# Optimization experiments

Measured on AMD Instinct MI355X. Metric: run time of the kernel, lower is better.

Reference implementation:

```python
import jax, jax.numpy as jnp
import numpy as np

N = 16384      # number of points (pixels)
C = 64         # value channels of U
D_REF = 5      # bilateral reference feature dim (xy + rgb)


def setup_inputs() -> dict:
    key = jax.random.key(0)
    k1, k2 = jax.random.split(key)
    U = jax.random.normal(k1, (N, C), dtype=jnp.float32)
    ref = jax.random.normal(k2, (N, D_REF), dtype=jnp.float32)
    return {"U": U, "ref": ref}


def reference(U, ref):
    # Gaussian filtering on reference features (exact form of the LSH-approx filter):
    #   out[i] = sum_j exp(-0.5 * ||ref_i - ref_j||^2) * U[j]  -  U[i]
    sq = jnp.sum(ref * ref, axis=-1)                      # [N]
    d2 = sq[:, None] + sq[None, :] - 2.0 * (ref @ ref.T)  # [N, N] squared distances
    K = jnp.exp(-0.5 * jnp.maximum(d2, 0.0))              # [N, N] Gaussian kernel
    return K @ U - U                                       # [N, C]
```

## Files before the change

### kernel.cpp

```cpp
#include <hip/hip_runtime.h>
#include <hip/hip_bf16.h>
#include <stdint.h>

#define N_PTS 16384
#define C_CH  64
#define D_REF 5
#define LOG2E 1.44269504088896340736f
#define IBLOCKS 64

typedef __attribute__((ext_vector_type(8))) short bf16x8;
typedef __attribute__((ext_vector_type(4))) float f32x4;

__device__ __forceinline__ unsigned short bf16rn(float v) {
    unsigned u = __builtin_bit_cast(unsigned, v) + 0x8000u;
    return (unsigned short)(u >> 16);
}
__device__ __forceinline__ float bf16tof(unsigned x) {
    return __builtin_bit_cast(float, x << 16);
}
__device__ __forceinline__ unsigned pack2bf16(float lo, float hi) {
    unsigned a = __builtin_bit_cast(unsigned, lo) + 0x8000u;
    unsigned b = __builtin_bit_cast(unsigned, hi) + 0x8000u;
    return __builtin_amdgcn_perm(b, a, 0x07060302u);
}
__device__ __forceinline__ unsigned cvt2(float lo, float hi) {
#if __has_builtin(__builtin_amdgcn_cvt_pk_bf16_f32)
    typedef __attribute__((ext_vector_type(2))) __bf16 bf162_t;
    bf162_t r = __builtin_amdgcn_cvt_pk_bf16_f32(lo, hi);
    return __builtin_bit_cast(unsigned, r);
#else
    return pack2bf16(lo, hi);
#endif
}
__device__ __forceinline__ float fast_exp2(float x) {
#if __has_builtin(__builtin_amdgcn_exp2f)
    return __builtin_amdgcn_exp2f(x);
#else
    return exp2f(x);
#endif
}

__device__ __forceinline__ void dma16(const unsigned short* g, unsigned short* l) {
#if __has_builtin(__builtin_amdgcn_global_load_lds)
    __builtin_amdgcn_global_load_lds(
        (const __attribute__((address_space(1))) unsigned int*)g,
        (__attribute__((address_space(3))) unsigned int*)l, 16, 0, 0);
#else
    const int lane = threadIdx.x & 63;
    *(uint4*)(l + lane * 8) = *(const uint4*)(g);
#endif
}

__global__ __launch_bounds__(256) void prep_all(
    const float* __restrict__ U, const float* __restrict__ ref,
    unsigned short* __restrict__ packA, unsigned short* __restrict__ packB,
    unsigned short* __restrict__ utPack)
{
    __shared__ unsigned short tile[64 * 80];
    const int bid = blockIdx.x;
    const int t   = threadIdx.x;

    if (bid < 512) {
        const int gid  = bid * 256 + t;
        const int half = gid >> 16;
        const int id   = gid & 0xFFFF;
        const int tile16 = id >> 6;
        const int lane = id & 63;
        const int q    = lane >> 4;
        const int m    = lane & 15;
        const int p = half ? (tile16 * 16 + m)
                           : ((tile16 >> 1) * 32 + (m >> 2) * 8 + (m & 3) + (tile16 & 1) * 4);

        const float* r = ref + (size_t)p * D_REF;
        float rv[5];
        float sq = 0.f;
#pragma unroll
        for (int d = 0; d < 5; ++d) { rv[d] = r[d]; sq += rv[d] * rv[d]; }
        const float h = -0.5f * LOG2E * sq;

        unsigned short bh[5], bl[5];
#pragma unroll
        for (int d = 0; d < 5; ++d) {
            const float base = half ? rv[d] * LOG2E : rv[d];
            bh[d] = bf16rn(base);
            bl[d] = bf16rn(base - bf16tof(bh[d]));
        }
        const unsigned short hh  = bf16rn(h);
        const unsigned short hl  = bf16rn(h - bf16tof(hh));
        const unsigned short one = 0x3F80;

        unsigned short outv[8];
#pragma unroll
        for (int tt = 0; tt < 8; ++tt) {
            const int k = q * 8 + tt;
            unsigned short v = 0;
            if (!half) {
                if      (k < 5)   v = bh[k];
                else if (k < 10)  v = bh[k - 5];
                else if (k < 15)  v = bl[k - 10];
                else if (k == 15) v = hh;
                else if (k == 16) v = hl;
                else if (k <= 18) v = one;
            } else {
                if      (k < 5)   v = bh[k];
                else if (k < 10)  v = bl[k - 5];
                else if (k < 15)  v = bh[k - 10];
                else if (k <= 16) v = one;
                else if (k == 17) v = hh;
                else if (k == 18) v = hl;
            }
            outv[tt] = v;
        }
        unsigned short* dst = (half ? packB : packA) + ((size_t)tile16 * 64 + lane) * 8;
        *(uint4*)dst = *(uint4*)outv;
    } else {
        const int b  = bid - 512;
        const int j0 = b * 64;
        const int c  = t & 63;
        const int jb = t >> 6;
#pragma unroll
        for (int k = 0; k < 16; ++k) {
            const int jr = jb + k * 4;
            tile[c * 80 + jr] = bf16rn(U[(size_t)(j0 + jr) * C_CH + c]);
        }
        __syncthreads();
#pragma unroll
        for (int rep = 0; rep < 2; ++rep) {
            const int id   = rep * 256 + t;
            const int lane = id & 63;
            const int ct   = (id >> 6) & 3;
            const int kt   = id >> 8;
            const int m    = lane & 15;
            const int q    = lane >> 4;
            const int cc   = ct * 16 + m;
            const int jloc = kt * 32 + q * 8;
            const uint4 frag = *(const uint4*)&tile[cc * 80 + jloc];
            const int jtile  = b * 2 + kt;
            *(uint4*)&utPack[(((size_t)jtile * 4 + ct) * 64 + lane) * 8] = frag;
        }
    }
}

template<int JS>
__global__ __launch_bounds__(256, 3) void lsh_main(
    const float* __restrict__ U,
    const unsigned short* __restrict__ packA,
    const unsigned short* __restrict__ packB,
    const unsigned short* __restrict__ utPack,
    unsigned short* __restrict__ part,
    float* __restrict__ out,
    int use_part)
{
    constexpr int UNITS  = (N_PTS / JS) / 32;
    constexpr int CUNITS = 8;
    constexpr int NCH    = UNITS / CUNITS;
    __shared__ __align__(16) unsigned short sh[CUNITS * 2048];

    const int t    = threadIdx.x;
    const int lane = t & 63;
    const int wave = t >> 6;
    const int q    = lane >> 4;
    const int m    = lane & 15;

    const int ib = blockIdx.x / JS;
    const int js = blockIdx.x % JS;

    bf16x8 bfrag[4];
#pragma unroll
    for (int s = 0; s < 4; ++s) {
        const int itile = ib * 16 + wave * 4 + s;
        bfrag[s] = *(const bf16x8*)(packB + ((size_t)itile * 64 + lane) * 8);
    }

    f32x4 acc[4][4];
#pragma unroll
    for (int s = 0; s < 4; ++s)
#pragma unroll
        for (int ct = 0; ct < 4; ++ct) acc[s][ct] = (f32x4){0.f, 0.f, 0.f, 0.f};

    const bf16x8 zero8 = {0, 0, 0, 0, 0, 0, 0, 0};
    bf16x8 cs0 = zero8, cs1 = zero8;
    bf16x8 uf[4] = {zero8, zero8, zero8, zero8};

    const unsigned short* pA = packA + ((size_t)js * UNITS) * 1024 + lane * 8;
    bf16x8 ga0 = *(const bf16x8*)pA;
    bf16x8 ga1 = *(const bf16x8*)(pA + 512);

    for (int ch = 0; ch < NCH; ++ch) {
        const unsigned short* srcU = utPack + (size_t)(js * UNITS + ch * CUNITS) * 2048;
        __syncthreads();
#pragma unroll
        for (int r = 0; r < CUNITS; ++r)
            dma16(srcU + (r * 4 + wave) * 512 + lane * 8, sh + (r * 4 + wave) * 512);
        __syncthreads();

#pragma unroll
        for (int u8 = 0; u8 < CUNITS; ++u8) {
            const f32x4 z = (f32x4){0.f, 0.f, 0.f, 0.f};
            f32x4 g0a = __builtin_amdgcn_mfma_f32_16x16x32_bf16(ga0, bfrag[0], z, 0, 0, 0);
            f32x4 g1a = __builtin_amdgcn_mfma_f32_16x16x32_bf16(ga1, bfrag[0], z, 0, 0, 0);
            f32x4 g0b = __builtin_amdgcn_mfma_f32_16x16x32_bf16(ga0, bfrag[1], z, 0, 0, 0);
            f32x4 g1b = __builtin_amdgcn_mfma_f32_16x16x32_bf16(ga1, bfrag[1], z, 0, 0, 0);
#pragma unroll
            for (int ct = 0; ct < 4; ++ct) {
                acc[2][ct] = __builtin_amdgcn_mfma_f32_16x16x32_bf16(uf[ct], cs0, acc[2][ct], 0, 0, 0);
                acc[3][ct] = __builtin_amdgcn_mfma_f32_16x16x32_bf16(uf[ct], cs1, acc[3][ct], 0, 0, 0);
            }
#pragma unroll
            for (int ct = 0; ct < 4; ++ct)
                uf[ct] = *(const bf16x8*)(sh + u8 * 2048 + ct * 512 + lane * 8);
            {
                union { unsigned u[4]; bf16x8 v; } sa, sb;
                sa.u[0] = cvt2(fast_exp2(g0a[0]), fast_exp2(g0a[1]));
                sa.u[1] = cvt2(fast_exp2(g0a[2]), fast_exp2(g0a[3]));
                sa.u[2] = cvt2(fast_exp2(g1a[0]), fast_exp2(g1a[1]));
                sa.u[3] = cvt2(fast_exp2(g1a[2]), fast_exp2(g1a[3]));
                sb.u[0] = cvt2(fast_exp2(g0b[0]), fast_exp2(g0b[1]));
                sb.u[1] = cvt2(fast_exp2(g0b[2]), fast_exp2(g0b[3]));
                sb.u[2] = cvt2(fast_exp2(g1b[0]), fast_exp2(g1b[1]));
                sb.u[3] = cvt2(fast_exp2(g1b[2]), fast_exp2(g1b[3]));
                cs0 = sa.v;
                cs1 = sb.v;
            }
            f32x4 h0a = __builtin_amdgcn_mfma_f32_16x16x32_bf16(ga0, bfrag[2], z, 0, 0, 0);
            f32x4 h1a = __builtin_amdgcn_mfma_f32_16x16x32_bf16(ga1, bfrag[2], z, 0, 0, 0);
            f32x4 h0b = __builtin_amdgcn_mfma_f32_16x16x32_bf16(ga0, bfrag[3], z, 0, 0, 0);
            f32x4 h1b = __builtin_amdgcn_mfma_f32_16x16x32_bf16(ga1, bfrag[3], z, 0, 0, 0);
#pragma unroll
            for (int ct = 0; ct < 4; ++ct) {
                acc[0][ct] = __builtin_amdgcn_mfma_f32_16x16x32_bf16(uf[ct], cs0, acc[0][ct], 0, 0, 0);
                acc[1][ct] = __builtin_amdgcn_mfma_f32_16x16x32_bf16(uf[ct], cs1, acc[1][ct], 0, 0, 0);
            }
            const bf16x8 nga0 = *(const bf16x8*)(pA + 1024);
            const bf16x8 nga1 = *(const bf16x8*)(pA + 1536);
            pA += 1024;
            {
                union { unsigned u[4]; bf16x8 v; } sa, sb;
                sa.u[0] = cvt2(fast_exp2(h0a[0]), fast_exp2(h0a[1]));
                sa.u[1] = cvt2(fast_exp2(h0a[2]), fast_exp2(h0a[3]));
                sa.u[2] = cvt2(fast_exp2(h1a[0]), fast_exp2(h1a[1]));
                sa.u[3] = cvt2(fast_exp2(h1a[2]), fast_exp2(h1a[3]));
                sb.u[0] = cvt2(fast_exp2(h0b[0]), fast_exp2(h0b[1]));
                sb.u[1] = cvt2(fast_exp2(h0b[2]), fast_exp2(h0b[3]));
                sb.u[2] = cvt2(fast_exp2(h1b[0]), fast_exp2(h1b[1]));
                sb.u[3] = cvt2(fast_exp2(h1b[2]), fast_exp2(h1b[3]));
                cs0 = sa.v;
                cs1 = sb.v;
            }
            ga0 = nga0;
            ga1 = nga1;
        }
    }
#pragma unroll
    for (int ct = 0; ct < 4; ++ct) {
        acc[2][ct] = __builtin_amdgcn_mfma_f32_16x16x32_bf16(uf[ct], cs0, acc[2][ct], 0, 0, 0);
        acc[3][ct] = __builtin_amdgcn_mfma_f32_16x16x32_bf16(uf[ct], cs1, acc[3][ct], 0, 0, 0);
    }

    if (use_part) {
        unsigned short* dst = part + ((size_t)js * IBLOCKS + ib) * 16384;
#pragma unroll
        for (int s = 0; s < 4; ++s)
#pragma unroll
            for (int cp = 0; cp < 2; ++cp) {
                uint4 w;
                w.x = cvt2(acc[s][cp*2+0][0], acc[s][cp*2+0][1]);
                w.y = cvt2(acc[s][cp*2+0][2], acc[s][cp*2+0][3]);
                w.z = cvt2(acc[s][cp*2+1][0], acc[s][cp*2+1][1]);
                w.w = cvt2(acc[s][cp*2+1][2], acc[s][cp*2+1][3]);
                *(uint4*)(dst + ((s * 2 + cp) * 256 + t) * 8) = w;
            }
    } else {
#pragma unroll
        for (int s = 0; s < 4; ++s) {
            const int i_glob = ib * 256 + (wave * 4 + s) * 16 + m;
#pragma unroll
            for (int ct = 0; ct < 4; ++ct)
#pragma unroll
                for (int r2 = 0; r2 < 4; ++r2) {
                    const int c = ct * 16 + q * 4 + r2;
                    float val = acc[s][ct][r2];
                    if (js == 0) val -= U[(size_t)i_glob * C_CH + c];
                    atomicAdd(&out[(size_t)i_glob * C_CH + c], val);
                }
        }
    }
}

template<int JS>
__global__ __launch_bounds__(256) void reduce_part(
    const unsigned short* __restrict__ part, const f32x4* __restrict__ Uv,
    f32x4* __restrict__ out)
{
    const int x  = blockIdx.x * 256 + threadIdx.x;
    const int i  = x >> 4;
    const int c4 = (x & 15) * 4;
    const int blk = i >> 8, il = i & 255;
    const int wv = il >> 6, s = (il >> 4) & 3, mm = il & 15;
    const int ct = c4 >> 4, qq = (c4 >> 2) & 3;
    const int cp = ct >> 1, cti = ct & 1;
    const size_t off = (size_t)blk * 16384 +
        (size_t)(((s * 2 + cp) * 256) + (wv * 64 + qq * 16 + mm)) * 8 + cti * 4;
    float s0 = 0.f, s1 = 0.f, s2 = 0.f, s3 = 0.f;
#pragma unroll
    for (int js = 0; js < JS; ++js) {
        const uint2 w = *(const uint2*)(part + (size_t)js * (IBLOCKS * 16384) + off);
        s0 += bf16tof(w.x & 0xFFFFu);
        s1 += bf16tof(w.x >> 16);
        s2 += bf16tof(w.y & 0xFFFFu);
        s3 += bf16tof(w.y >> 16);
    }
    const f32x4 u = Uv[x];
    out[x] = (f32x4){s0 - u[0], s1 - u[1], s2 - u[2], s3 - u[3]};
}

extern "C" void kernel_launch(void* const* d_in, const int* in_sizes, int n_in,
                              void* d_out, int out_size, void* d_ws, size_t ws_size,
                              hipStream_t stream) {
    const float* U   = (const float*)d_in[0];
    const float* ref = (const float*)d_in[1];
    float* out = (float*)d_out;

    unsigned short* utPack = (unsigned short*)d_ws;
    unsigned short* packA  = (unsigned short*)((char*)d_ws + (size_t)2 * 1024 * 1024);
    unsigned short* packB  = (unsigned short*)((char*)d_ws + (size_t)3 * 1024 * 1024);
    unsigned short* part   = (unsigned short*)((char*)d_ws + (size_t)4 * 1024 * 1024);

    const size_t MB = 1024 * 1024;
    prep_all<<<768, 256, 0, stream>>>(U, ref, packA, packB, utPack);

    if (ws_size >= (4 + 2 * 16) * MB) {
        lsh_main<16><<<IBLOCKS * 16, 256, 0, stream>>>(U, packA, packB, utPack,
                                                       part, out, 1);
        reduce_part<16><<<1024, 256, 0, stream>>>(part, (const f32x4*)U, (f32x4*)out);
    } else {
        hipMemsetAsync(d_out, 0, (size_t)out_size * sizeof(float), stream);
        lsh_main<8><<<IBLOCKS * 8, 256, 0, stream>>>(U, packA, packB, utPack,
                                                     part, out, 0);
    }
}
```

Before: 124.1 us.

## Fuse split-K partial reduction into main kernel via last-block atomic counter

```diff
diff --git a/kernel.cpp b/kernel.cpp
--- a/kernel.cpp
+++ b/kernel.cpp
@@ -39,7 +39,6 @@
     return exp2f(x);
 #endif
 }
-
 __device__ __forceinline__ void dma16(const unsigned short* g, unsigned short* l) {
 #if __has_builtin(__builtin_amdgcn_global_load_lds)
     __builtin_amdgcn_global_load_lds(
@@ -54,11 +53,13 @@
 __global__ __launch_bounds__(256) void prep_all(
     const float* __restrict__ U, const float* __restrict__ ref,
     unsigned short* __restrict__ packA, unsigned short* __restrict__ packB,
-    unsigned short* __restrict__ utPack)
+    unsigned short* __restrict__ utPack, int* __restrict__ cnt)
 {
     __shared__ unsigned short tile[64 * 80];
     const int bid = blockIdx.x;
     const int t   = threadIdx.x;
+
+    if (bid == 0 && t < IBLOCKS) cnt[t] = 0;
 
     if (bid < 512) {
         const int gid  = bid * 256 + t;
@@ -132,9 +133,7 @@
             const int kt   = id >> 8;
             const int m    = lane & 15;
             const int q    = lane >> 4;
-            const int cc   = ct * 16 + m;
-            const int jloc = kt * 32 + q * 8;
-            const uint4 frag = *(const uint4*)&tile[cc * 80 + jloc];
+            const uint4 frag = *(const uint4*)&tile[(ct * 16 + m) * 80 + kt * 32 + q * 8];
             const int jtile  = b * 2 + kt;
             *(uint4*)&utPack[(((size_t)jtile * 4 + ct) * 64 + lane) * 8] = frag;
         }
@@ -148,6 +147,7 @@
     const unsigned short* __restrict__ packB,
     const unsigned short* __restrict__ utPack,
     unsigned short* __restrict__ part,
+    int* __restrict__ cnt,
     float* __restrict__ out,
     int use_part)
 {
@@ -155,6 +155,7 @@
     constexpr int CUNITS = 8;
     constexpr int NCH    = UNITS / CUNITS;
     __shared__ __align__(16) unsigned short sh[CUNITS * 2048];
+    __shared__ int lastFlag;
 
     const int t    = threadIdx.x;
     const int lane = t & 63;
@@ -270,6 +271,42 @@
                 w.w = cvt2(acc[s][cp*2+1][2], acc[s][cp*2+1][3]);
                 *(uint4*)(dst + ((s * 2 + cp) * 256 + t) * 8) = w;
             }
+
+        __syncthreads();
+        if (t == 0) {
+            __threadfence();
+            lastFlag = (atomicAdd(&cnt[ib], 1) == JS - 1) ? 1 : 0;
+        }
+        __syncthreads();
+        if (lastFlag) {
+            __threadfence();
+#pragma unroll
+            for (int s = 0; s < 4; ++s)
+#pragma unroll
+                for (int cp = 0; cp < 2; ++cp) {
+                    float v[8];
+#pragma unroll
+                    for (int k = 0; k < 8; ++k) v[k] = 0.f;
+                    const int row = s * 2 + cp;
+                    for (int j2 = 0; j2 < JS; ++j2) {
+                        const uint4 w = *(const uint4*)(part
+                            + ((size_t)j2 * IBLOCKS + ib) * 16384
+                            + (row * 256 + t) * 8);
+                        v[0] += bf16tof(w.x & 0xFFFFu); v[1] += bf16tof(w.x >> 16);
+                        v[2] += bf16tof(w.y & 0xFFFFu); v[3] += bf16tof(w.y >> 16);
+                        v[4] += bf16tof(w.z & 0xFFFFu); v[5] += bf16tof(w.z >> 16);
+                        v[6] += bf16tof(w.w & 0xFFFFu); v[7] += bf16tof(w.w >> 16);
+                    }
+                    const int i_glob = ib * 256 + (wave * 4 + s) * 16 + m;
+#pragma unroll
+                    for (int h = 0; h < 2; ++h) {
+                        const size_t o = (size_t)i_glob * C_CH + (cp * 2 + h) * 16 + q * 4;
+                        const f32x4 uv = *(const f32x4*)(U + o);
+                        *(f32x4*)(out + o) = (f32x4){v[h*4+0] - uv[0], v[h*4+1] - uv[1],
+                                                     v[h*4+2] - uv[2], v[h*4+3] - uv[3]};
+                    }
+                }
+        }
     } else {
 #pragma unroll
         for (int s = 0; s < 4; ++s) {
@@ -287,33 +324,6 @@
     }
 }
 
-template<int JS>
-__global__ __launch_bounds__(256) void reduce_part(
-    const unsigned short* __restrict__ part, const f32x4* __restrict__ Uv,
-    f32x4* __restrict__ out)
-{
-    const int x  = blockIdx.x * 256 + threadIdx.x;
-    const int i  = x >> 4;
-    const int c4 = (x & 15) * 4;
-    const int blk = i >> 8, il = i & 255;
-    const int wv = il >> 6, s = (il >> 4) & 3, mm = il & 15;
-    const int ct = c4 >> 4, qq = (c4 >> 2) & 3;
-    const int cp = ct >> 1, cti = ct & 1;
-    const size_t off = (size_t)blk * 16384 +
-        (size_t)(((s * 2 + cp) * 256) + (wv * 64 + qq * 16 + mm)) * 8 + cti * 4;
-    float s0 = 0.f, s1 = 0.f, s2 = 0.f, s3 = 0.f;
-#pragma unroll
-    for (int js = 0; js < JS; ++js) {
-        const uint2 w = *(const uint2*)(part + (size_t)js * (IBLOCKS * 16384) + off);
-        s0 += bf16tof(w.x & 0xFFFFu);
-        s1 += bf16tof(w.x >> 16);
-        s2 += bf16tof(w.y & 0xFFFFu);
-        s3 += bf16tof(w.y >> 16);
-    }
-    const f32x4 u = Uv[x];
-    out[x] = (f32x4){s0 - u[0], s1 - u[1], s2 - u[2], s3 - u[3]};
-}
-
 extern "C" void kernel_launch(void* const* d_in, const int* in_sizes, int n_in,
                               void* d_out, int out_size, void* d_ws, size_t ws_size,
                               hipStream_t stream) {
@@ -325,17 +335,17 @@
     unsigned short* packA  = (unsigned short*)((char*)d_ws + (size_t)2 * 1024 * 1024);
     unsigned short* packB  = (unsigned short*)((char*)d_ws + (size_t)3 * 1024 * 1024);
     unsigned short* part   = (unsigned short*)((char*)d_ws + (size_t)4 * 1024 * 1024);
+    int*            cnt    = (int*)((char*)d_ws + (size_t)36 * 1024 * 1024);
 
     const size_t MB = 1024 * 1024;
-    prep_all<<<768, 256, 0, stream>>>(U, ref, packA, packB, utPack);
-
-    if (ws_size >= (4 + 2 * 16) * MB) {
+    prep_all<<<768, 256, 0, stream>>>(U, ref, packA, packB, utPack, cnt);
+
+    if (ws_size >= 37 * MB) {
         lsh_main<16><<<IBLOCKS * 16, 256, 0, stream>>>(U, packA, packB, utPack,
-                                                       part, out, 1);
-        reduce_part<16><<<1024, 256, 0, stream>>>(part, (const f32x4*)U, (f32x4*)out);
+                                                       part, cnt, out, 1);
     } else {
         hipMemsetAsync(d_out, 0, (size_t)out_size * sizeof(float), stream);
         lsh_main<8><<<IBLOCKS * 8, 256, 0, stream>>>(U, packA, packB, utPack,
-                                                     part, out, 0);
-    }
-}
+                                                     part, cnt, out, 0);
+    }
+}
```

Result: slower. 225.5 us (+81.7%).

## Double-buffer U tiles in LDS and drop software-pipelined exp staging

Applied to the files above, without the earlier changes.

```diff
diff --git a/kernel.cpp b/kernel.cpp
--- a/kernel.cpp
+++ b/kernel.cpp
@@ -39,7 +39,6 @@
     return exp2f(x);
 #endif
 }
-
 __device__ __forceinline__ void dma16(const unsigned short* g, unsigned short* l) {
 #if __has_builtin(__builtin_amdgcn_global_load_lds)
     __builtin_amdgcn_global_load_lds(
@@ -83,10 +82,10 @@
         for (int d = 0; d < 5; ++d) {
             const float base = half ? rv[d] * LOG2E : rv[d];
             bh[d] = bf16rn(base);
-            bl[d] = bf16rn(base - bf16tof(bh[d]));
+            bl[d] = bf16rn(base - bf16tof((unsigned)bh[d]));
         }
         const unsigned short hh  = bf16rn(h);
-        const unsigned short hl  = bf16rn(h - bf16tof(hh));
+        const unsigned short hl  = bf16rn(h - bf16tof((unsigned)hh));
         const unsigned short one = 0x3F80;
 
         unsigned short outv[8];
@@ -132,9 +131,7 @@
             const int kt   = id >> 8;
             const int m    = lane & 15;
             const int q    = lane >> 4;
-            const int cc   = ct * 16 + m;
-            const int jloc = kt * 32 + q * 8;
-            const uint4 frag = *(const uint4*)&tile[cc * 80 + jloc];
+            const uint4 frag = *(const uint4*)&tile[(ct * 16 + m) * 80 + kt * 32 + q * 8];
             const int jtile  = b * 2 + kt;
             *(uint4*)&utPack[(((size_t)jtile * 4 + ct) * 64 + lane) * 8] = frag;
         }
@@ -142,7 +139,7 @@
 }
 
 template<int JS>
-__global__ __launch_bounds__(256, 3) void lsh_main(
+__global__ __launch_bounds__(256, 4) void lsh_main(
     const float* __restrict__ U,
     const unsigned short* __restrict__ packA,
     const unsigned short* __restrict__ packB,
@@ -152,9 +149,9 @@
     int use_part)
 {
     constexpr int UNITS  = (N_PTS / JS) / 32;
-    constexpr int CUNITS = 8;
+    constexpr int CUNITS = 4;
     constexpr int NCH    = UNITS / CUNITS;
-    __shared__ __align__(16) unsigned short sh[CUNITS * 2048];
+    __shared__ __align__(16) unsigned short sh[2 * CUNITS * 2048];
 
     const int t    = threadIdx.x;
     const int lane = t & 63;
@@ -178,38 +175,39 @@
 #pragma unroll
         for (int ct = 0; ct < 4; ++ct) acc[s][ct] = (f32x4){0.f, 0.f, 0.f, 0.f};
 
-    const bf16x8 zero8 = {0, 0, 0, 0, 0, 0, 0, 0};
-    bf16x8 cs0 = zero8, cs1 = zero8;
-    bf16x8 uf[4] = {zero8, zero8, zero8, zero8};
-
     const unsigned short* pA = packA + ((size_t)js * UNITS) * 1024 + lane * 8;
     bf16x8 ga0 = *(const bf16x8*)pA;
     bf16x8 ga1 = *(const bf16x8*)(pA + 512);
 
+    const unsigned short* srcU0 = utPack + ((size_t)js * UNITS) * 2048;
+#pragma unroll
+    for (int r = 0; r < CUNITS; ++r)
+        dma16(srcU0 + (r * 4 + wave) * 512 + lane * 8, sh + (r * 4 + wave) * 512);
+    __syncthreads();
+
     for (int ch = 0; ch < NCH; ++ch) {
-        const unsigned short* srcU = utPack + (size_t)(js * UNITS + ch * CUNITS) * 2048;
-        __syncthreads();
-#pragma unroll
-        for (int r = 0; r < CUNITS; ++r)
-            dma16(srcU + (r * 4 + wave) * 512 + lane * 8, sh + (r * 4 + wave) * 512);
-        __syncthreads();
-
-#pragma unroll
-        for (int u8 = 0; u8 < CUNITS; ++u8) {
+        unsigned short* buf = sh + (ch & 1) * (CUNITS * 2048);
+        if (ch + 1 < NCH) {
+            const unsigned short* srcN = srcU0 + (size_t)(ch + 1) * (CUNITS * 2048);
+            unsigned short* nbuf = sh + ((ch + 1) & 1) * (CUNITS * 2048);
+#pragma unroll
+            for (int r = 0; r < CUNITS; ++r)
+                dma16(srcN + (r * 4 + wave) * 512 + lane * 8, nbuf + (r * 4 + wave) * 512);
+        }
+
+#pragma unroll
+        for (int u4 = 0; u4 < CUNITS; ++u4) {
+            const bf16x8 nga0 = *(const bf16x8*)(pA + 1024);
+            const bf16x8 nga1 = *(const bf16x8*)(pA + 1536);
+
             const f32x4 z = (f32x4){0.f, 0.f, 0.f, 0.f};
-            f32x4 g0a = __builtin_amdgcn_mfma_f32_16x16x32_bf16(ga0, bfrag[0], z, 0, 0, 0);
-            f32x4 g1a = __builtin_amdgcn_mfma_f32_16x16x32_bf16(ga1, bfrag[0], z, 0, 0, 0);
-            f32x4 g0b = __builtin_amdgcn_mfma_f32_16x16x32_bf16(ga0, bfrag[1], z, 0, 0, 0);
-            f32x4 g1b = __builtin_amdgcn_mfma_f32_16x16x32_bf16(ga1, bfrag[1], z, 0, 0, 0);
-#pragma unroll
-            for (int ct = 0; ct < 4; ++ct) {
-                acc[2][ct] = __builtin_amdgcn_mfma_f32_16x16x32_bf16(uf[ct], cs0, acc[2][ct], 0, 0, 0);
-                acc[3][ct] = __builtin_amdgcn_mfma_f32_16x16x32_bf16(uf[ct], cs1, acc[3][ct], 0, 0, 0);
-            }
-#pragma unroll
-            for (int ct = 0; ct < 4; ++ct)
-                uf[ct] = *(const bf16x8*)(sh + u8 * 2048 + ct * 512 + lane * 8);
-            {
+            bf16x8 sfrag[4];
+#pragma unroll
+            for (int sp = 0; sp < 2; ++sp) {
+                f32x4 g0a = __builtin_amdgcn_mfma_f32_16x16x32_bf16(ga0, bfrag[sp*2+0], z, 0, 0, 0);
+                f32x4 g1a = __builtin_amdgcn_mfma_f32_16x16x32_bf16(ga1, bfrag[sp*2+0], z, 0, 0, 0);
+                f32x4 g0b = __builtin_amdgcn_mfma_f32_16x16x32_bf16(ga0, bfrag[sp*2+1], z, 0, 0, 0);
+                f32x4 g1b = __builtin_amdgcn_mfma_f32_16x16x32_bf16(ga1, bfrag[sp*2+1], z, 0, 0, 0);
                 union { unsigned u[4]; bf16x8 v; } sa, sb;
                 sa.u[0] = cvt2(fast_exp2(g0a[0]), fast_exp2(g0a[1]));
                 sa.u[1] = cvt2(fast_exp2(g0a[2]), fast_exp2(g0a[3]));
@@ -219,42 +217,22 @@
                 sb.u[1] = cvt2(fast_exp2(g0b[2]), fast_exp2(g0b[3]));
                 sb.u[2] = cvt2(fast_exp2(g1b[0]), fast_exp2(g1b[1]));
                 sb.u[3] = cvt2(fast_exp2(g1b[2]), fast_exp2(g1b[3]));
-                cs0 = sa.v;
-                cs1 = sb.v;
+                sfrag[sp*2+0] = sa.v;
+                sfrag[sp*2+1] = sb.v;
             }
-            f32x4 h0a = __builtin_amdgcn_mfma_f32_16x16x32_bf16(ga0, bfrag[2], z, 0, 0, 0);
-            f32x4 h1a = __builtin_amdgcn_mfma_f32_16x16x32_bf16(ga1, bfrag[2], z, 0, 0, 0);
-            f32x4 h0b = __builtin_amdgcn_mfma_f32_16x16x32_bf16(ga0, bfrag[3], z, 0, 0, 0);
-            f32x4 h1b = __builtin_amdgcn_mfma_f32_16x16x32_bf16(ga1, bfrag[3], z, 0, 0, 0);
 #pragma unroll
             for (int ct = 0; ct < 4; ++ct) {
-                acc[0][ct] = __builtin_amdgcn_mfma_f32_16x16x32_bf16(uf[ct], cs0, acc[0][ct], 0, 0, 0);
-                acc[1][ct] = __builtin_amdgcn_mfma_f32_16x16x32_bf16(uf[ct], cs1, acc[1][ct], 0, 0, 0);
+                const bf16x8 uf = *(const bf16x8*)(buf + u4 * 2048 + ct * 512 + lane * 8);
+#pragma unroll
+                for (int s = 0; s < 4; ++s)
+                    acc[s][ct] = __builtin_amdgcn_mfma_f32_16x16x32_bf16(
+                        uf, sfrag[s], acc[s][ct], 0, 0, 0);
             }
-            const bf16x8 nga0 = *(const bf16x8*)(pA + 1024);
-            const bf16x8 nga1 = *(const bf16x8*)(pA + 1536);
             pA += 1024;
-            {
-                union { unsigned u[4]; bf16x8 v; } sa, sb;
-                sa.u[0] = cvt2(fast_exp2(h0a[0]), fast_exp2(h0a[1]));
-                sa.u[1] = cvt2(fast_exp2(h0a[2]), fast_exp2(h0a[3]));
-                sa.u[2] = cvt2(fast_exp2(h1a[0]), fast_exp2(h1a[1]));
-                sa.u[3] = cvt2(fast_exp2(h1a[2]), fast_exp2(h1a[3]));
-                sb.u[0] = cvt2(fast_exp2(h0b[0]), fast_exp2(h0b[1]));
-                sb.u[1] = cvt2(fast_exp2(h0b[2]), fast_exp2(h0b[3]));
-                sb.u[2] = cvt2(fast_exp2(h1b[0]), fast_exp2(h1b[1]));
-                sb.u[3] = cvt2(fast_exp2(h1b[2]), fast_exp2(h1b[3]));
-                cs0 = sa.v;
-                cs1 = sb.v;
-            }
             ga0 = nga0;
             ga1 = nga1;
         }
-    }
-#pragma unroll
-    for (int ct = 0; ct < 4; ++ct) {
-        acc[2][ct] = __builtin_amdgcn_mfma_f32_16x16x32_bf16(uf[ct], cs0, acc[2][ct], 0, 0, 0);
-        acc[3][ct] = __builtin_amdgcn_mfma_f32_16x16x32_bf16(uf[ct], cs1, acc[3][ct], 0, 0, 0);
+        __syncthreads();
     }
 
     if (use_part) {
@@ -329,7 +307,7 @@
     const size_t MB = 1024 * 1024;
     prep_all<<<768, 256, 0, stream>>>(U, ref, packA, packB, utPack);
 
-    if (ws_size >= (4 + 2 * 16) * MB) {
+    if (ws_size >= 36 * MB) {
         lsh_main<16><<<IBLOCKS * 16, 256, 0, stream>>>(U, packA, packB, utPack,
                                                        part, out, 1);
         reduce_part<16><<<1024, 256, 0, stream>>>(part, (const f32x4*)U, (f32x4*)out);
```

Measured after the change: 137.1 us. +10.5%, slower.
